# Kernel tuning notes

Measured on AMD Instinct MI355X. Metric: run time of the kernel, lower is better.

The kernel has to match this reference:

```python
import jax, jax.numpy as jnp
import numpy as np

N = 50000
E = 800000
D = 128
L = 2


def setup_inputs() -> dict:
    key = jax.random.key(0)
    k0, k1, k2 = jax.random.split(key, 3)
    x = jax.random.normal(k0, (N, D), dtype=jnp.float32)
    edge_index = jax.random.randint(k1, (2, E), 0, N, dtype=jnp.int64)
    # GCNConv weights: one [D, D] matrix + bias per layer (dim_in -> dim_in)
    W = jax.random.normal(k2, (L, D, D), dtype=jnp.float32) * (1.0 / np.sqrt(D))
    b = jnp.zeros((L, D), dtype=jnp.float32)
    return {"x": x, "edge_index": edge_index, "W": W, "b": b}


def reference(x, edge_index, W, b):
    """Stacked GCNConv + relu (dropout is identity in eval mode).

    GCNConv: out = D^{-1/2} (A + I) D^{-1/2} (X W) + b, with self-loops added.
    """
    n = x.shape[0]
    loops = jnp.arange(n, dtype=edge_index.dtype)
    src = jnp.concatenate([edge_index[0], loops])  # [E + N]
    dst = jnp.concatenate([edge_index[1], loops])  # [E + N]
    # Degree (with self-loops) based symmetric normalization
    deg = jax.ops.segment_sum(jnp.ones_like(dst, dtype=x.dtype), dst, num_segments=n)
    dinv = jax.lax.rsqrt(deg)  # deg >= 1 thanks to self-loops
    coef = (dinv[src] * dinv[dst])[:, None]  # [E + N, 1]

    num_layers = W.shape[0]
    for i in range(num_layers):
        h = x @ W[i]  # transform first, as PyG GCNConv does
        x = jax.ops.segment_sum(h[src] * coef, dst, num_segments=n) + b[i]
        x = jax.nn.relu(x)
        # F.dropout with training=False is identity
    return x
```

## Files before the change

### kernel.cpp

```cpp
#include <hip/hip_runtime.h>
#include <hip/hip_fp16.h>


#define D 128
#define SCAN_B 256
#define WP 136
#define ABI 6

typedef _Float16 half8 __attribute__((ext_vector_type(8)));
typedef float floatx4 __attribute__((ext_vector_type(4)));


__global__ void count_kernel(const int* __restrict__ dst, int* deg8,
                             int* __restrict__ rank, int e, int n) {
    int i = blockIdx.x * blockDim.x + threadIdx.x;
    int c = (blockIdx.x & 7) * n;
    if (i < e) rank[i] = atomicAdd(&deg8[c + dst[i]], 1);
}

__global__ __launch_bounds__(256) void scanA_cvtw_kernel(const int* __restrict__ deg8,
                                                         int* __restrict__ degT,
                                                         int* __restrict__ base8,
                                                         int* __restrict__ partial,
                                                         int n, int nbs,
                                                         const float* __restrict__ W,
                                                         __half* __restrict__ WhT) {
    __shared__ int red[4];
    int tid = threadIdx.x;
    int bid = blockIdx.x;
    if (bid < nbs) {
        int i = bid * 256 + tid;
        int tot = 0;
        if (i < n) {
            int run = 0;
#pragma unroll
            for (int c = 0; c < 8; ++c) {
                base8[c * n + i] = run;
                run += deg8[c * n + i];
            }
            degT[i] = run;
            tot = run;
        }
        for (int off = 32; off > 0; off >>= 1) tot += __shfl_down(tot, off, 64);
        if ((tid & 63) == 0) red[tid >> 6] = tot;
        __syncthreads();
        if (tid == 0) partial[bid] = red[0] + red[1] + red[2] + red[3];
    } else {
        int id = (bid - nbs) * 256 + tid;
        int l = id >> 14;
        int rem = id & 16383;
        int f = rem >> 7;
        int k = rem & 127;
        WhT[id] = __float2half(W[l * 16384 + k * 128 + f]);
    }
}

__global__ __launch_bounds__(256) void scanB_kernel(const int* __restrict__ partial,
                                                    int* __restrict__ blockoff, int nb) {
    __shared__ int sc[256];
    int tid = threadIdx.x;
    int c = (tid < nb) ? partial[tid] : 0;
    sc[tid] = c;
    __syncthreads();
    for (int off = 1; off < 256; off <<= 1) {
        int v = (tid >= off) ? sc[tid - off] : 0;
        __syncthreads();
        sc[tid] += v;
        __syncthreads();
    }
    if (tid <= nb) blockoff[tid] = (tid == 0) ? 0 : sc[tid - 1];
}

__global__ __launch_bounds__(SCAN_B) void scanC_kernel(const int* __restrict__ degT,
                                                       const int* __restrict__ blockoff,
                                                       int* __restrict__ row_ptr,
                                                       float* __restrict__ dinv,
                                                       int n, int nb) {
    __shared__ int sc[SCAN_B];
    int tid = threadIdx.x;
    int i = blockIdx.x * SCAN_B + tid;
    int c = (i < n) ? degT[i] : 0;
    sc[tid] = c;
    __syncthreads();
    for (int off = 1; off < SCAN_B; off <<= 1) {
        int v = (tid >= off) ? sc[tid - off] : 0;
        __syncthreads();
        sc[tid] += v;
        __syncthreads();
    }
    if (i < n) {
        int base = blockoff[blockIdx.x] + sc[tid] - c;
        row_ptr[i] = base;
        dinv[i] = rsqrtf((float)(c + 1));
    }
    if (blockIdx.x == 0 && tid == 0) row_ptr[n] = blockoff[nb];
}


__device__ inline void gemm_body(int bid, int tid,
                                 const float* __restrict__ Xf,
                                 const __half* __restrict__ Xh,
                                 const __half* __restrict__ WhT,
                                 __half* __restrict__ Hh, int n, int fromFloat,
                                 _Float16* wlds) {
#pragma unroll
    for (int q = 0; q < 8; ++q) {
        int idx = tid + q * 256;
        int row = idx >> 4;
        int col8 = (idx & 15) * 8;
        const uint2* gsrc = (const uint2*)(WhT + row * 128 + col8);
        uint2 a = gsrc[0];
        uint2 b = gsrc[1];
        uint2* ldst = (uint2*)(wlds + row * WP + col8);
        ldst[0] = a;
        ldst[1] = b;
    }
    __syncthreads();

    const int wave = tid >> 6;
    const int lane = tid & 63;
    const int m = lane & 15;
    const int quad = lane >> 4;

    const int node = bid * 64 + wave * 16 + m;
    const int node_ld = node < n ? node : (n - 1);

    half8 bfr[4];
    if (fromFloat) {
#pragma unroll
        for (int k = 0; k < 4; ++k) {
            const float4* p = (const float4*)(Xf + (size_t)node_ld * 128 + k * 32 + quad * 8);
            float4 lo = p[0];
            float4 hi = p[1];
            half8 h;
            h[0] = (_Float16)lo.x; h[1] = (_Float16)lo.y;
            h[2] = (_Float16)lo.z; h[3] = (_Float16)lo.w;
            h[4] = (_Float16)hi.x; h[5] = (_Float16)hi.y;
            h[6] = (_Float16)hi.z; h[7] = (_Float16)hi.w;
            bfr[k] = h;
        }
    } else {
#pragma unroll
        for (int k = 0; k < 4; ++k) {
            bfr[k] = *(const half8*)(Xh + (size_t)node_ld * 128 + k * 32 + quad * 8);
        }
    }

    floatx4 acc[8];
#pragma unroll
    for (int f = 0; f < 8; ++f) acc[f] = (floatx4){0.f, 0.f, 0.f, 0.f};

#pragma unroll
    for (int f = 0; f < 8; ++f) {
#pragma unroll
        for (int k = 0; k < 4; ++k) {
            half8 a = *(const half8*)(wlds + (f * 16 + m) * WP + k * 32 + quad * 8);
            acc[f] = __builtin_amdgcn_mfma_f32_16x16x32_f16(a, bfr[k], acc[f], 0, 0, 0);
        }
    }

    if (node < n) {
#pragma unroll
        for (int f = 0; f < 8; ++f) {
            __half2 p0 = __floats2half2_rn(acc[f][0], acc[f][1]);
            __half2 p1 = __floats2half2_rn(acc[f][2], acc[f][3]);
            uint2 pk;
            pk.x = *(unsigned int*)&p0;
            pk.y = *(unsigned int*)&p1;
            *(uint2*)(Hh + (size_t)node * 128 + f * 16 + quad * 4) = pk;
        }
    }
}

__device__ inline void fill_body(int i,
                                 const int* __restrict__ src,
                                 const int* __restrict__ dst,
                                 const int* __restrict__ rank,
                                 const int* __restrict__ row_ptr,
                                 const int* __restrict__ base8,
                                 const float* __restrict__ dinv,
                                 int2* __restrict__ recs, int e, int n) {
    if (i < e) {
        int d = dst[i];
        int s = src[i];
        int c = (i >> 8) & 7;
        int pos = row_ptr[d] + base8[c * n + d] + rank[i];
        int2 rec;
        rec.x = s;
        rec.y = __float_as_int(dinv[s] * dinv[d]);
        recs[pos] = rec;
    }
}


__global__ __launch_bounds__(256) void gemmfill_kernel(const float* __restrict__ Xf,
                                                       const __half* __restrict__ WhT,
                                                       __half* __restrict__ Hh, int n, int nbg,
                                                       const int* __restrict__ src,
                                                       const int* __restrict__ dst,
                                                       const int* __restrict__ rank,
                                                       const int* __restrict__ row_ptr,
                                                       const int* __restrict__ base8,
                                                       const float* __restrict__ dinv,
                                                       int2* __restrict__ recs, int e) {
    __shared__ _Float16 wlds[128 * WP];
    int bid = blockIdx.x;
    int tid = threadIdx.x;
    if (bid < nbg) {
        gemm_body(bid, tid, Xf, nullptr, WhT, Hh, n, 1, wlds);
    } else {
        fill_body((bid - nbg) * 256 + tid, src, dst, rank, row_ptr, base8, dinv, recs, e, n);
    }
}

__global__ __launch_bounds__(256) void gemm_f16in_kernel(const __half* __restrict__ Xh,
                                                         const __half* __restrict__ WhT,
                                                         __half* __restrict__ Hh, int n) {
    __shared__ _Float16 wlds[128 * WP];
    gemm_body(blockIdx.x, threadIdx.x, nullptr, Xh, WhT, Hh, n, 0, wlds);
}


__device__ inline void unpack8(uint4 u, float* f) {
    union { unsigned int x; __half2 h; } a, b, c, d;
    a.x = u.x; b.x = u.y; c.x = u.z; d.x = u.w;
    float2 f0 = __half22float2(a.h);
    float2 f1 = __half22float2(b.h);
    float2 f2 = __half22float2(c.h);
    float2 f3 = __half22float2(d.h);
    f[0] = f0.x; f[1] = f0.y; f[2] = f1.x; f[3] = f1.y;
    f[4] = f2.x; f[5] = f2.y; f[6] = f3.x; f[7] = f3.y;
}

__global__ __launch_bounds__(256) void agg_kernel(const __half* __restrict__ H,
                                                  const int2* __restrict__ recs,
                                                  const int* __restrict__ row_ptr,
                                                  const float* __restrict__ dinv,
                                                  const float* __restrict__ bias,
                                                  float* __restrict__ YF,
                                                  __half* __restrict__ YH,
                                                  int n, int writeHalf) {
    int wave = threadIdx.x >> 6;
    int lane = threadIdx.x & 63;
    int v = blockIdx.x * 4 + wave;
    if (v >= n) return;

    const int qw = lane >> 4;
    const int fl = lane & 15;
    const uint4* H16 = (const uint4*)H;

    float acc[8];
    {
        float di = dinv[v];
        float selfc = (qw == 0) ? di * di : 0.f;
        uint4 hv = H16[(size_t)v * 16 + fl];
        float f[8]; unpack8(hv, f);
#pragma unroll
        for (int t = 0; t < 8; ++t) acc[t] = f[t] * selfc;
    }

    int e0 = row_ptr[v];
    int e1 = row_ptr[v + 1];
    int e = e0;
    for (; e + 4 * ABI <= e1; e += 4 * ABI) {
        int2 r[ABI]; uint4 hu[ABI];
#pragma unroll
        for (int j = 0; j < ABI; ++j) r[j] = recs[e + 4 * j + qw];
#pragma unroll
        for (int j = 0; j < ABI; ++j) hu[j] = H16[(size_t)r[j].x * 16 + fl];
#pragma unroll
        for (int j = 0; j < ABI; ++j) {
            float c = __int_as_float(r[j].y);
            float f[8]; unpack8(hu[j], f);
#pragma unroll
            for (int t = 0; t < 8; ++t) acc[t] = fmaf(f[t], c, acc[t]);
        }
    }
    if (e < e1) {
        int2 r[ABI]; uint4 hu[ABI]; bool act[ABI];
#pragma unroll
        for (int j = 0; j < ABI; ++j) {
            int idx = e + 4 * j + qw;
            act[j] = idx < e1;
            if (act[j]) r[j] = recs[idx];
        }
#pragma unroll
        for (int j = 0; j < ABI; ++j) {
            if (act[j]) hu[j] = H16[(size_t)r[j].x * 16 + fl];
        }
#pragma unroll
        for (int j = 0; j < ABI; ++j) {
            if (act[j]) {
                float c = __int_as_float(r[j].y);
                float f[8]; unpack8(hu[j], f);
#pragma unroll
                for (int t = 0; t < 8; ++t) acc[t] = fmaf(f[t], c, acc[t]);
            }
        }
    }

#pragma unroll
    for (int t = 0; t < 8; ++t) {
        acc[t] += __shfl_xor(acc[t], 16);
        acc[t] += __shfl_xor(acc[t], 32);
    }

    if (qw == 0) {
        const float4* B4 = (const float4*)bias;
        float4 b0 = B4[fl * 2];
        float4 b1 = B4[fl * 2 + 1];
        float o[8];
        o[0] = fmaxf(acc[0] + b0.x, 0.f);
        o[1] = fmaxf(acc[1] + b0.y, 0.f);
        o[2] = fmaxf(acc[2] + b0.z, 0.f);
        o[3] = fmaxf(acc[3] + b0.w, 0.f);
        o[4] = fmaxf(acc[4] + b1.x, 0.f);
        o[5] = fmaxf(acc[5] + b1.y, 0.f);
        o[6] = fmaxf(acc[6] + b1.z, 0.f);
        o[7] = fmaxf(acc[7] + b1.w, 0.f);
        if (writeHalf) {
            __half2 p0 = __floats2half2_rn(o[0], o[1]);
            __half2 p1 = __floats2half2_rn(o[2], o[3]);
            __half2 p2 = __floats2half2_rn(o[4], o[5]);
            __half2 p3 = __floats2half2_rn(o[6], o[7]);
            uint4 pk;
            pk.x = *(unsigned int*)&p0;
            pk.y = *(unsigned int*)&p1;
            pk.z = *(unsigned int*)&p2;
            pk.w = *(unsigned int*)&p3;
            ((uint4*)YH)[(size_t)v * 16 + fl] = pk;
        } else {
            float4* Y4 = (float4*)YF;
            Y4[(size_t)v * 32 + fl * 2]     = make_float4(o[0], o[1], o[2], o[3]);
            Y4[(size_t)v * 32 + fl * 2 + 1] = make_float4(o[4], o[5], o[6], o[7]);
        }
    }
}


extern "C" void kernel_launch(void* const* d_in, const int* in_sizes, int n_in,
                              void* d_out, int out_size, void* d_ws, size_t ws_size,
                              hipStream_t stream) {
    const float* x = (const float*)d_in[0];
    const int* ei = (const int*)d_in[1];
    const float* W = (const float*)d_in[2];
    const float* b = (const float*)d_in[3];
    float* out = (float*)d_out;

    const int N = in_sizes[0] / D;
    const int E = in_sizes[1] / 2;

    const int* src = ei;
    const int* dst = ei + E;

    int* wsi = (int*)d_ws;
    float* wsf = (float*)d_ws;
    const size_t o_deg8 = 0;
    const size_t o_degT = o_deg8 + 400000;
    const size_t o_dinv = o_degT + 50000;
    const size_t o_rp   = o_dinv + 50000;
    const size_t o_part = o_rp + 50016;
    const size_t o_boff = o_part + 256;
    const size_t o_b8   = o_boff + 256;
    const size_t o_rank = o_b8 + 400000;
    const size_t o_rec  = o_rank + 800000;
    const size_t o_h    = o_rec + 1600000;
    const size_t o_wht  = o_h + 3200000;
    const size_t o_y1h  = o_wht + 16384;

    int* deg8    = wsi + o_deg8;
    int* degT    = wsi + o_degT;
    float* dinv  = wsf + o_dinv;
    int* row_ptr = wsi + o_rp;
    int* partial = wsi + o_part;
    int* blockoff= wsi + o_boff;
    int* base8   = wsi + o_b8;
    int* rank    = wsi + o_rank;
    int2* recs   = (int2*)(wsi + o_rec);
    __half* h    = (__half*)(wsi + o_h);
    __half* wht  = (__half*)(wsi + o_wht);
    __half* y1h  = (__half*)(wsi + o_y1h);

    const int nb_e = (E + 255) / 256;
    const int nb_s = (N + SCAN_B - 1) / SCAN_B;
    const int nb_g = (N + 63) / 64;
    const int nb_a = (N + 3) / 4;

    hipMemsetAsync(deg8, 0, (size_t)8 * 50000 * sizeof(int), stream);
    count_kernel<<<nb_e, 256, 0, stream>>>(dst, deg8, rank, E, N);
    scanA_cvtw_kernel<<<nb_s + 128, 256, 0, stream>>>(deg8, degT, base8, partial,
                                                      N, nb_s, W, wht);
    scanB_kernel<<<1, 256, 0, stream>>>(partial, blockoff, nb_s);
    scanC_kernel<<<nb_s, SCAN_B, 0, stream>>>(degT, blockoff, row_ptr, dinv, N, nb_s);
    gemmfill_kernel<<<nb_g + nb_e, 256, 0, stream>>>(x, wht, h, N, nb_g,
                                                     src, dst, rank, row_ptr, base8,
                                                     dinv, recs, E);
    agg_kernel<<<nb_a, 256, 0, stream>>>(h, recs, row_ptr, dinv, b, nullptr, y1h, N, 1);
    gemm_f16in_kernel<<<nb_g, 256, 0, stream>>>(y1h, wht + 16384, h, N);
    agg_kernel<<<nb_a, 256, 0, stream>>>(h, recs, row_ptr, dinv, b + D, out, nullptr, N, 0);
}
```

Measured before the change: 237.5 us.

## Fuse count, scans, and GEMM/fill into one persistent kernel with grid barriers

Replaces the count, three scan kernels and the gemm+fill kernel with a single persistent prep kernel of fixed grid size that uses atomic-counter grid barriers between phases. This removes four kernel launches and their inter-kernel gaps, and folds the block-offset scan into each block redundantly. It relies on all 768 blocks being co-resident (launch bounds 256,3) to avoid deadlock, and the GEMM and fill phases now loop over tiles with fewer blocks.

```diff
diff --git a/kernel.cpp b/kernel.cpp
--- a/kernel.cpp
+++ b/kernel.cpp
@@ -3,106 +3,29 @@
 
 
 #define D 128
-#define SCAN_B 256
 #define WP 136
 #define ABI 6
+#define GRID_PREP 768
+#define GB_G 384
+#define NB_SCAN 196
 
 typedef _Float16 half8 __attribute__((ext_vector_type(8)));
 typedef float floatx4 __attribute__((ext_vector_type(4)));
 
-
-__global__ void count_kernel(const int* __restrict__ dst, int* deg8,
-                             int* __restrict__ rank, int e, int n) {
-    int i = blockIdx.x * blockDim.x + threadIdx.x;
-    int c = (blockIdx.x & 7) * n;
-    if (i < e) rank[i] = atomicAdd(&deg8[c + dst[i]], 1);
-}
-
-__global__ __launch_bounds__(256) void scanA_cvtw_kernel(const int* __restrict__ deg8,
-                                                         int* __restrict__ degT,
-                                                         int* __restrict__ base8,
-                                                         int* __restrict__ partial,
-                                                         int n, int nbs,
-                                                         const float* __restrict__ W,
-                                                         __half* __restrict__ WhT) {
-    __shared__ int red[4];
-    int tid = threadIdx.x;
-    int bid = blockIdx.x;
-    if (bid < nbs) {
-        int i = bid * 256 + tid;
-        int tot = 0;
-        if (i < n) {
-            int run = 0;
-#pragma unroll
-            for (int c = 0; c < 8; ++c) {
-                base8[c * n + i] = run;
-                run += deg8[c * n + i];
-            }
-            degT[i] = run;
-            tot = run;
-        }
-        for (int off = 32; off > 0; off >>= 1) tot += __shfl_down(tot, off, 64);
-        if ((tid & 63) == 0) red[tid >> 6] = tot;
-        __syncthreads();
-        if (tid == 0) partial[bid] = red[0] + red[1] + red[2] + red[3];
-    } else {
-        int id = (bid - nbs) * 256 + tid;
-        int l = id >> 14;
-        int rem = id & 16383;
-        int f = rem >> 7;
-        int k = rem & 127;
-        WhT[id] = __float2half(W[l * 16384 + k * 128 + f]);
-    }
-}
-
-__global__ __launch_bounds__(256) void scanB_kernel(const int* __restrict__ partial,
-                                                    int* __restrict__ blockoff, int nb) {
-    __shared__ int sc[256];
-    int tid = threadIdx.x;
-    int c = (tid < nb) ? partial[tid] : 0;
-    sc[tid] = c;
+__device__ inline void gsync(int* ctr, int target) {
     __syncthreads();
-    for (int off = 1; off < 256; off <<= 1) {
-        int v = (tid >= off) ? sc[tid - off] : 0;
-        __syncthreads();
-        sc[tid] += v;
-        __syncthreads();
-    }
-    if (tid <= nb) blockoff[tid] = (tid == 0) ? 0 : sc[tid - 1];
-}
-
-__global__ __launch_bounds__(SCAN_B) void scanC_kernel(const int* __restrict__ degT,
-                                                       const int* __restrict__ blockoff,
-                                                       int* __restrict__ row_ptr,
-                                                       float* __restrict__ dinv,
-                                                       int n, int nb) {
-    __shared__ int sc[SCAN_B];
-    int tid = threadIdx.x;
-    int i = blockIdx.x * SCAN_B + tid;
-    int c = (i < n) ? degT[i] : 0;
-    sc[tid] = c;
+    if (threadIdx.x == 0) {
+        __threadfence();
+        atomicAdd(ctr, 1);
+        while (__hip_atomic_load(ctr, __ATOMIC_RELAXED, __HIP_MEMORY_SCOPE_AGENT) < target)
+            __builtin_amdgcn_s_sleep(2);
+        __threadfence();
+    }
     __syncthreads();
-    for (int off = 1; off < SCAN_B; off <<= 1) {
-        int v = (tid >= off) ? sc[tid - off] : 0;
-        __syncthreads();
-        sc[tid] += v;
-        __syncthreads();
-    }
-    if (i < n) {
-        int base = blockoff[blockIdx.x] + sc[tid] - c;
-        row_ptr[i] = base;
-        dinv[i] = rsqrtf((float)(c + 1));
-    }
-    if (blockIdx.x == 0 && tid == 0) row_ptr[n] = blockoff[nb];
-}
-
-
-__device__ inline void gemm_body(int bid, int tid,
-                                 const float* __restrict__ Xf,
-                                 const __half* __restrict__ Xh,
-                                 const __half* __restrict__ WhT,
-                                 __half* __restrict__ Hh, int n, int fromFloat,
-                                 _Float16* wlds) {
+}
+
+
+__device__ inline void stage_w(int tid, const __half* __restrict__ WhT, _Float16* wlds) {
 #pragma unroll
     for (int q = 0; q < 8; ++q) {
         int idx = tid + q * 256;
@@ -115,14 +38,19 @@
         ldst[0] = a;
         ldst[1] = b;
     }
-    __syncthreads();
-
+}
+
+__device__ inline void gemm_tile(int g, int tid,
+                                 const float* __restrict__ Xf,
+                                 const __half* __restrict__ Xh,
+                                 __half* __restrict__ Hh, int n, int fromFloat,
+                                 const _Float16* wlds) {
     const int wave = tid >> 6;
     const int lane = tid & 63;
     const int m = lane & 15;
     const int quad = lane >> 4;
 
-    const int node = bid * 64 + wave * 16 + m;
+    const int node = g * 64 + wave * 16 + m;
     const int node_ld = node < n ? node : (n - 1);
 
     half8 bfr[4];
@@ -170,6 +98,17 @@
             *(uint2*)(Hh + (size_t)node * 128 + f * 16 + quad * 4) = pk;
         }
     }
+}
+
+__device__ inline void gemm_body(int bid, int tid,
+                                 const float* __restrict__ Xf,
+                                 const __half* __restrict__ Xh,
+                                 const __half* __restrict__ WhT,
+                                 __half* __restrict__ Hh, int n, int fromFloat,
+                                 _Float16* wlds) {
+    stage_w(tid, WhT, wlds);
+    __syncthreads();
+    gemm_tile(bid, tid, Xf, Xh, Hh, n, fromFloat, wlds);
 }
 
 __device__ inline void fill_body(int i,
@@ -193,25 +132,92 @@
 }
 
 
-__global__ __launch_bounds__(256) void gemmfill_kernel(const float* __restrict__ Xf,
-                                                       const __half* __restrict__ WhT,
-                                                       __half* __restrict__ Hh, int n, int nbg,
-                                                       const int* __restrict__ src,
-                                                       const int* __restrict__ dst,
-                                                       const int* __restrict__ rank,
-                                                       const int* __restrict__ row_ptr,
-                                                       const int* __restrict__ base8,
-                                                       const float* __restrict__ dinv,
-                                                       int2* __restrict__ recs, int e) {
+__global__ __launch_bounds__(256, 3) void prep_kernel(
+    const int* __restrict__ src, const int* __restrict__ dst,
+    const float* __restrict__ x, const float* __restrict__ W,
+    int* __restrict__ deg8, int* __restrict__ base8,
+    int* __restrict__ partial,
+    int* __restrict__ row_ptr, float* __restrict__ dinv,
+    int* __restrict__ rank, int2* __restrict__ recs,
+    __half* __restrict__ WhT, __half* __restrict__ Hh,
+    int* ctr, int n, int e, int nbg) {
     __shared__ _Float16 wlds[128 * WP];
-    int bid = blockIdx.x;
-    int tid = threadIdx.x;
-    if (bid < nbg) {
-        gemm_body(bid, tid, Xf, nullptr, WhT, Hh, n, 1, wlds);
+    __shared__ int sc[256];
+    __shared__ int scb[256];
+    const int tid = threadIdx.x;
+    const int bid = blockIdx.x;
+    const int gid = bid * 256 + tid;
+
+    if (gid < 2 * D * D) {
+        int l = gid >> 14;
+        int rem = gid & 16383;
+        int f = rem >> 7;
+        int k = rem & 127;
+        WhT[gid] = __float2half(W[l * 16384 + k * 128 + f]);
+    }
+    for (int i = gid; i < e; i += GRID_PREP * 256) {
+        int c = (i >> 8) & 7;
+        rank[i] = atomicAdd(&deg8[c * n + dst[i]], 1);
+    }
+    gsync(ctr, GRID_PREP);
+
+    int mydeg = 0, myscan = 0;
+    if (bid < NB_SCAN) {
+        int i = gid;
+        if (i < n) {
+            int run = 0;
+#pragma unroll
+            for (int c = 0; c < 8; ++c) {
+                base8[c * n + i] = run;
+                run += deg8[c * n + i];
+            }
+            mydeg = run;
+        }
+        sc[tid] = mydeg;
+        __syncthreads();
+        for (int off = 1; off < 256; off <<= 1) {
+            int v = (tid >= off) ? sc[tid - off] : 0;
+            __syncthreads();
+            sc[tid] += v;
+            __syncthreads();
+        }
+        myscan = sc[tid];
+        if (tid == 255) partial[bid] = myscan;
+    }
+    gsync(ctr, 2 * GRID_PREP);
+
+    if (bid < NB_SCAN) {
+        int p = (tid < NB_SCAN) ? partial[tid] : 0;
+        scb[tid] = p;
+        __syncthreads();
+        for (int off = 1; off < 256; off <<= 1) {
+            int v = (tid >= off) ? scb[tid - off] : 0;
+            __syncthreads();
+            scb[tid] += v;
+            __syncthreads();
+        }
+        int boff = (bid == 0) ? 0 : scb[bid - 1];
+        int i = gid;
+        if (i < n) {
+            row_ptr[i] = boff + myscan - mydeg;
+            dinv[i] = rsqrtf((float)(mydeg + 1));
+        }
+        if (bid == 0 && tid == 0) row_ptr[n] = scb[NB_SCAN - 1];
+    }
+    gsync(ctr, 3 * GRID_PREP);
+
+    if (bid < GB_G) {
+        stage_w(tid, WhT, wlds);
+        __syncthreads();
+        for (int g = bid; g < nbg; g += GB_G)
+            gemm_tile(g, tid, x, nullptr, Hh, n, 1, wlds);
     } else {
-        fill_body((bid - nbg) * 256 + tid, src, dst, rank, row_ptr, base8, dinv, recs, e, n);
-    }
-}
+        const int FB = GRID_PREP - GB_G;
+        for (int i = (bid - GB_G) * 256 + tid; i < e; i += FB * 256)
+            fill_body(i, src, dst, rank, row_ptr, base8, dinv, recs, e, n);
+    }
+}
+
 
 __global__ __launch_bounds__(256) void gemm_f16in_kernel(const __half* __restrict__ Xh,
                                                          const __half* __restrict__ WhT,
@@ -356,12 +362,11 @@
     int* wsi = (int*)d_ws;
     float* wsf = (float*)d_ws;
     const size_t o_deg8 = 0;
-    const size_t o_degT = o_deg8 + 400000;
-    const size_t o_dinv = o_degT + 50000;
+    const size_t o_ctr  = o_deg8 + 400000;
+    const size_t o_dinv = o_ctr + 16;
     const size_t o_rp   = o_dinv + 50000;
     const size_t o_part = o_rp + 50016;
-    const size_t o_boff = o_part + 256;
-    const size_t o_b8   = o_boff + 256;
+    const size_t o_b8   = o_part + 256;
     const size_t o_rank = o_b8 + 400000;
     const size_t o_rec  = o_rank + 800000;
     const size_t o_h    = o_rec + 1600000;
@@ -369,11 +374,10 @@
     const size_t o_y1h  = o_wht + 16384;
 
     int* deg8    = wsi + o_deg8;
-    int* degT    = wsi + o_degT;
+    int* ctr     = wsi + o_ctr;
     float* dinv  = wsf + o_dinv;
     int* row_ptr = wsi + o_rp;
     int* partial = wsi + o_part;
-    int* blockoff= wsi + o_boff;
     int* base8   = wsi + o_b8;
     int* rank    = wsi + o_rank;
     int2* recs   = (int2*)(wsi + o_rec);
@@ -381,20 +385,13 @@
     __half* wht  = (__half*)(wsi + o_wht);
     __half* y1h  = (__half*)(wsi + o_y1h);
 
-    const int nb_e = (E + 255) / 256;
-    const int nb_s = (N + SCAN_B - 1) / SCAN_B;
     const int nb_g = (N + 63) / 64;
     const int nb_a = (N + 3) / 4;
 
-    hipMemsetAsync(deg8, 0, (size_t)8 * 50000 * sizeof(int), stream);
-    count_kernel<<<nb_e, 256, 0, stream>>>(dst, deg8, rank, E, N);
-    scanA_cvtw_kernel<<<nb_s + 128, 256, 0, stream>>>(deg8, degT, base8, partial,
-                                                      N, nb_s, W, wht);
-    scanB_kernel<<<1, 256, 0, stream>>>(partial, blockoff, nb_s);
-    scanC_kernel<<<nb_s, SCAN_B, 0, stream>>>(degT, blockoff, row_ptr, dinv, N, nb_s);
-    gemmfill_kernel<<<nb_g + nb_e, 256, 0, stream>>>(x, wht, h, N, nb_g,
-                                                     src, dst, rank, row_ptr, base8,
-                                                     dinv, recs, E);
+    hipMemsetAsync(deg8, 0, (size_t)(8 * 50000 + 16) * sizeof(int), stream);
+    prep_kernel<<<GRID_PREP, 256, 0, stream>>>(src, dst, x, W,
+                                               deg8, base8, partial, row_ptr, dinv,
+                                               rank, recs, wht, h, ctr, N, E, nb_g);
     agg_kernel<<<nb_a, 256, 0, stream>>>(h, recs, row_ptr, dinv, b, nullptr, y1h, N, 1);
     gemm_f16in_kernel<<<nb_g, 256, 0, stream>>>(y1h, wht + 16384, h, N);
     agg_kernel<<<nb_a, 256, 0, stream>>>(h, recs, row_ptr, dinv, b + D, out, nullptr, N, 0);
```

Measured after the change: 455.4 us. 1.92x slower.

## Fuse layer-1 aggregation with layer-2 GEMM and merge scan kernels

Applied to the files above, without the earlier changes.

Layer-1 aggregation and the layer-2 transform now run in one kernel. Each 512-thread block aggregates 64 nodes into an LDS tile and immediately multiplies it by the second weight matrix with MFMA. This removes the fp16 intermediate write/read round trip and one launch. Separately, the two-stage block-offset scan is folded into the row-pointer kernel, which hardcodes 196 scan blocks (valid only for N=50000) and saves another launch. The fused kernel serializes 8 rows per wave and reads the weights straight from global memory, so the aggregation may lose latency hiding.

```diff
diff --git a/kernel.cpp b/kernel.cpp
--- a/kernel.cpp
+++ b/kernel.cpp
@@ -3,9 +3,10 @@
 
 
 #define D 128
-#define SCAN_B 256
 #define WP 136
+#define YP 136
 #define ABI 6
+#define NB_SCAN 196
 
 typedef _Float16 half8 __attribute__((ext_vector_type(8)));
 typedef float floatx4 __attribute__((ext_vector_type(4)));
@@ -55,11 +56,25 @@
     }
 }
 
-__global__ __launch_bounds__(256) void scanB_kernel(const int* __restrict__ partial,
-                                                    int* __restrict__ blockoff, int nb) {
+__global__ __launch_bounds__(256) void scanC2_kernel(const int* __restrict__ degT,
+                                                     const int* __restrict__ partial,
+                                                     int* __restrict__ row_ptr,
+                                                     float* __restrict__ dinv, int n) {
     __shared__ int sc[256];
+    __shared__ int scb[256];
     int tid = threadIdx.x;
-    int c = (tid < nb) ? partial[tid] : 0;
+    int bid = blockIdx.x;
+    int p = (tid < NB_SCAN) ? partial[tid] : 0;
+    scb[tid] = p;
+    __syncthreads();
+    for (int off = 1; off < 256; off <<= 1) {
+        int v = (tid >= off) ? scb[tid - off] : 0;
+        __syncthreads();
+        scb[tid] += v;
+        __syncthreads();
+    }
+    int i = bid * 256 + tid;
+    int c = (i < n) ? degT[i] : 0;
     sc[tid] = c;
     __syncthreads();
     for (int off = 1; off < 256; off <<= 1) {
@@ -68,40 +83,19 @@
         sc[tid] += v;
         __syncthreads();
     }
-    if (tid <= nb) blockoff[tid] = (tid == 0) ? 0 : sc[tid - 1];
-}
-
-__global__ __launch_bounds__(SCAN_B) void scanC_kernel(const int* __restrict__ degT,
-                                                       const int* __restrict__ blockoff,
-                                                       int* __restrict__ row_ptr,
-                                                       float* __restrict__ dinv,
-                                                       int n, int nb) {
-    __shared__ int sc[SCAN_B];
-    int tid = threadIdx.x;
-    int i = blockIdx.x * SCAN_B + tid;
-    int c = (i < n) ? degT[i] : 0;
-    sc[tid] = c;
-    __syncthreads();
-    for (int off = 1; off < SCAN_B; off <<= 1) {
-        int v = (tid >= off) ? sc[tid - off] : 0;
-        __syncthreads();
-        sc[tid] += v;
-        __syncthreads();
-    }
     if (i < n) {
-        int base = blockoff[blockIdx.x] + sc[tid] - c;
+        int base = ((bid == 0) ? 0 : scb[bid - 1]) + sc[tid] - c;
         row_ptr[i] = base;
         dinv[i] = rsqrtf((float)(c + 1));
     }
-    if (blockIdx.x == 0 && tid == 0) row_ptr[n] = blockoff[nb];
+    if (bid == 0 && tid == 0) row_ptr[n] = scb[NB_SCAN - 1];
 }
 
 
 __device__ inline void gemm_body(int bid, int tid,
                                  const float* __restrict__ Xf,
-                                 const __half* __restrict__ Xh,
                                  const __half* __restrict__ WhT,
-                                 __half* __restrict__ Hh, int n, int fromFloat,
+                                 __half* __restrict__ Hh, int n,
                                  _Float16* wlds) {
 #pragma unroll
     for (int q = 0; q < 8; ++q) {
@@ -126,24 +120,17 @@
     const int node_ld = node < n ? node : (n - 1);
 
     half8 bfr[4];
-    if (fromFloat) {
-#pragma unroll
-        for (int k = 0; k < 4; ++k) {
-            const float4* p = (const float4*)(Xf + (size_t)node_ld * 128 + k * 32 + quad * 8);
-            float4 lo = p[0];
-            float4 hi = p[1];
-            half8 h;
-            h[0] = (_Float16)lo.x; h[1] = (_Float16)lo.y;
-            h[2] = (_Float16)lo.z; h[3] = (_Float16)lo.w;
-            h[4] = (_Float16)hi.x; h[5] = (_Float16)hi.y;
-            h[6] = (_Float16)hi.z; h[7] = (_Float16)hi.w;
-            bfr[k] = h;
-        }
-    } else {
-#pragma unroll
-        for (int k = 0; k < 4; ++k) {
-            bfr[k] = *(const half8*)(Xh + (size_t)node_ld * 128 + k * 32 + quad * 8);
-        }
+#pragma unroll
+    for (int k = 0; k < 4; ++k) {
+        const float4* p = (const float4*)(Xf + (size_t)node_ld * 128 + k * 32 + quad * 8);
+        float4 lo = p[0];
+        float4 hi = p[1];
+        half8 h;
+        h[0] = (_Float16)lo.x; h[1] = (_Float16)lo.y;
+        h[2] = (_Float16)lo.z; h[3] = (_Float16)lo.w;
+        h[4] = (_Float16)hi.x; h[5] = (_Float16)hi.y;
+        h[6] = (_Float16)hi.z; h[7] = (_Float16)hi.w;
+        bfr[k] = h;
     }
 
     floatx4 acc[8];
@@ -207,17 +194,10 @@
     int bid = blockIdx.x;
     int tid = threadIdx.x;
     if (bid < nbg) {
-        gemm_body(bid, tid, Xf, nullptr, WhT, Hh, n, 1, wlds);
+        gemm_body(bid, tid, Xf, WhT, Hh, n, wlds);
     } else {
         fill_body((bid - nbg) * 256 + tid, src, dst, rank, row_ptr, base8, dinv, recs, e, n);
     }
-}
-
-__global__ __launch_bounds__(256) void gemm_f16in_kernel(const __half* __restrict__ Xh,
-                                                         const __half* __restrict__ WhT,
-                                                         __half* __restrict__ Hh, int n) {
-    __shared__ _Float16 wlds[128 * WP];
-    gemm_body(blockIdx.x, threadIdx.x, nullptr, Xh, WhT, Hh, n, 0, wlds);
 }
 
 
@@ -232,14 +212,68 @@
     f[4] = f2.x; f[5] = f2.y; f[6] = f3.x; f[7] = f3.y;
 }
 
+__device__ inline void agg_row(int v, int qw, int fl,
+                               const uint4* __restrict__ H16,
+                               const int2* __restrict__ recs,
+                               const int* __restrict__ row_ptr,
+                               const float* __restrict__ dinv,
+                               float* acc) {
+    {
+        float di = dinv[v];
+        float selfc = (qw == 0) ? di * di : 0.f;
+        uint4 hv = H16[(size_t)v * 16 + fl];
+        float f[8]; unpack8(hv, f);
+#pragma unroll
+        for (int t = 0; t < 8; ++t) acc[t] = f[t] * selfc;
+    }
+
+    int e0 = row_ptr[v];
+    int e1 = row_ptr[v + 1];
+    int e = e0;
+    for (; e + 4 * ABI <= e1; e += 4 * ABI) {
+        int2 r[ABI]; uint4 hu[ABI];
+#pragma unroll
+        for (int j = 0; j < ABI; ++j) r[j] = recs[e + 4 * j + qw];
+#pragma unroll
+        for (int j = 0; j < ABI; ++j) hu[j] = H16[(size_t)r[j].x * 16 + fl];
+#pragma unroll
+        for (int j = 0; j < ABI; ++j) {
+            float c = __int_as_float(r[j].y);
+            float f[8]; unpack8(hu[j], f);
+#pragma unroll
+            for (int t = 0; t < 8; ++t) acc[t] = fmaf(f[t], c, acc[t]);
+        }
+    }
+    if (e < e1) {
+        int2 r[ABI]; uint4 hu[ABI]; bool act[ABI];
+#pragma unroll
+        for (int j = 0; j < ABI; ++j) {
+            int idx = e + 4 * j + qw;
+            act[j] = idx < e1;
+            if (act[j]) r[j] = recs[idx];
+        }
+#pragma unroll
+        for (int j = 0; j < ABI; ++j) {
+            if (act[j]) hu[j] = H16[(size_t)r[j].x * 16 + fl];
+        }
+#pragma unroll
+        for (int j = 0; j < ABI; ++j) {
+            if (act[j]) {
+                float c = __int_as_float(r[j].y);
+                float f[8]; unpack8(hu[j], f);
+#pragma unroll
+                for (int t = 0; t < 8; ++t) acc[t] = fmaf(f[t], c, acc[t]);
+            }
+        }
+    }
+}
+
 __global__ __launch_bounds__(256) void agg_kernel(const __half* __restrict__ H,
                                                   const int2* __restrict__ recs,
                                                   const int* __restrict__ row_ptr,
                                                   const float* __restrict__ dinv,
                                                   const float* __restrict__ bias,
-                                                  float* __restrict__ YF,
-                                                  __half* __restrict__ YH,
-                                                  int n, int writeHalf) {
+                                                  float* __restrict__ YF, int n) {
     int wave = threadIdx.x >> 6;
     int lane = threadIdx.x & 63;
     int v = blockIdx.x * 4 + wave;
@@ -250,54 +284,7 @@
     const uint4* H16 = (const uint4*)H;
 
     float acc[8];
-    {
-        float di = dinv[v];
-        float selfc = (qw == 0) ? di * di : 0.f;
-        uint4 hv = H16[(size_t)v * 16 + fl];
-        float f[8]; unpack8(hv, f);
-#pragma unroll
-        for (int t = 0; t < 8; ++t) acc[t] = f[t] * selfc;
-    }
-
-    int e0 = row_ptr[v];
-    int e1 = row_ptr[v + 1];
-    int e = e0;
-    for (; e + 4 * ABI <= e1; e += 4 * ABI) {
-        int2 r[ABI]; uint4 hu[ABI];
-#pragma unroll
-        for (int j = 0; j < ABI; ++j) r[j] = recs[e + 4 * j + qw];
-#pragma unroll
-        for (int j = 0; j < ABI; ++j) hu[j] = H16[(size_t)r[j].x * 16 + fl];
-#pragma unroll
-        for (int j = 0; j < ABI; ++j) {
-            float c = __int_as_float(r[j].y);
-            float f[8]; unpack8(hu[j], f);
-#pragma unroll
-            for (int t = 0; t < 8; ++t) acc[t] = fmaf(f[t], c, acc[t]);
-        }
-    }
-    if (e < e1) {
-        int2 r[ABI]; uint4 hu[ABI]; bool act[ABI];
-#pragma unroll
-        for (int j = 0; j < ABI; ++j) {
-            int idx = e + 4 * j + qw;
-            act[j] = idx < e1;
-            if (act[j]) r[j] = recs[idx];
-        }
-#pragma unroll
-        for (int j = 0; j < ABI; ++j) {
-            if (act[j]) hu[j] = H16[(size_t)r[j].x * 16 + fl];
-        }
-#pragma unroll
-        for (int j = 0; j < ABI; ++j) {
-            if (act[j]) {
-                float c = __int_as_float(r[j].y);
-                float f[8]; unpack8(hu[j], f);
-#pragma unroll
-                for (int t = 0; t < 8; ++t) acc[t] = fmaf(f[t], c, acc[t]);
-            }
-        }
-    }
+    agg_row(v, qw, fl, H16, recs, row_ptr, dinv, acc);
 
 #pragma unroll
     for (int t = 0; t < 8; ++t) {
@@ -309,30 +296,92 @@
         const float4* B4 = (const float4*)bias;
         float4 b0 = B4[fl * 2];
         float4 b1 = B4[fl * 2 + 1];
-        float o[8];
-        o[0] = fmaxf(acc[0] + b0.x, 0.f);
-        o[1] = fmaxf(acc[1] + b0.y, 0.f);
-        o[2] = fmaxf(acc[2] + b0.z, 0.f);
-        o[3] = fmaxf(acc[3] + b0.w, 0.f);
-        o[4] = fmaxf(acc[4] + b1.x, 0.f);
-        o[5] = fmaxf(acc[5] + b1.y, 0.f);
-        o[6] = fmaxf(acc[6] + b1.z, 0.f);
-        o[7] = fmaxf(acc[7] + b1.w, 0.f);
-        if (writeHalf) {
-            __half2 p0 = __floats2half2_rn(o[0], o[1]);
-            __half2 p1 = __floats2half2_rn(o[2], o[3]);
-            __half2 p2 = __floats2half2_rn(o[4], o[5]);
-            __half2 p3 = __floats2half2_rn(o[6], o[7]);
-            uint4 pk;
+        float4* Y4 = (float4*)YF;
+        Y4[(size_t)v * 32 + fl * 2] = make_float4(
+            fmaxf(acc[0] + b0.x, 0.f), fmaxf(acc[1] + b0.y, 0.f),
+            fmaxf(acc[2] + b0.z, 0.f), fmaxf(acc[3] + b0.w, 0.f));
+        Y4[(size_t)v * 32 + fl * 2 + 1] = make_float4(
+            fmaxf(acc[4] + b1.x, 0.f), fmaxf(acc[5] + b1.y, 0.f),
+            fmaxf(acc[6] + b1.z, 0.f), fmaxf(acc[7] + b1.w, 0.f));
+    }
+}
+
+__global__ __launch_bounds__(512, 4) void aggemm_kernel(
+    const __half* __restrict__ H,
+    const int2* __restrict__ recs,
+    const int* __restrict__ row_ptr,
+    const float* __restrict__ dinv,
+    const float* __restrict__ bias,
+    const __half* __restrict__ WhT2,
+    __half* __restrict__ H2, int n) {
+    __shared__ _Float16 yt[64 * YP];
+    const int tid = threadIdx.x;
+    const int wave = tid >> 6;
+    const int lane = tid & 63;
+    const int qw = lane >> 4;
+    const int fl = lane & 15;
+    const int g = blockIdx.x;
+    const uint4* H16 = (const uint4*)H;
+
+    const float4* B4 = (const float4*)bias;
+    float4 b0 = B4[fl * 2];
+    float4 b1 = B4[fl * 2 + 1];
+#pragma unroll 1
+    for (int it = 0; it < 8; ++it) {
+        int r = wave * 8 + it;
+        int v = g * 64 + r;
+        if (v < n) {
+            float acc[8];
+            agg_row(v, qw, fl, H16, recs, row_ptr, dinv, acc);
+#pragma unroll
+            for (int t = 0; t < 8; ++t) {
+                acc[t] += __shfl_xor(acc[t], 16);
+                acc[t] += __shfl_xor(acc[t], 32);
+            }
+            if (qw == 0) {
+                __half2 p0 = __floats2half2_rn(fmaxf(acc[0] + b0.x, 0.f), fmaxf(acc[1] + b0.y, 0.f));
+                __half2 p1 = __floats2half2_rn(fmaxf(acc[2] + b0.z, 0.f), fmaxf(acc[3] + b0.w, 0.f));
+                __half2 p2 = __floats2half2_rn(fmaxf(acc[4] + b1.x, 0.f), fmaxf(acc[5] + b1.y, 0.f));
+                __half2 p3 = __floats2half2_rn(fmaxf(acc[6] + b1.z, 0.f), fmaxf(acc[7] + b1.w, 0.f));
+                uint4 pk;
+                pk.x = *(unsigned int*)&p0;
+                pk.y = *(unsigned int*)&p1;
+                pk.z = *(unsigned int*)&p2;
+                pk.w = *(unsigned int*)&p3;
+                *(uint4*)&yt[r * YP + fl * 8] = pk;
+            }
+        } else if (qw == 0) {
+            uint4 z = make_uint4(0, 0, 0, 0);
+            *(uint4*)&yt[r * YP + fl * 8] = z;
+        }
+    }
+    __syncthreads();
+
+    const int mg = wave & 3;
+    const int fh = wave >> 2;
+    const int node = g * 64 + mg * 16 + fl;
+
+    half8 bfr[4];
+#pragma unroll
+    for (int k = 0; k < 4; ++k)
+        bfr[k] = *(const half8*)&yt[(mg * 16 + fl) * YP + k * 32 + qw * 8];
+
+#pragma unroll
+    for (int fb = 0; fb < 4; ++fb) {
+        int f = fh * 4 + fb;
+        floatx4 a4 = (floatx4){0.f, 0.f, 0.f, 0.f};
+#pragma unroll
+        for (int k = 0; k < 4; ++k) {
+            half8 a = *(const half8*)(WhT2 + ((f * 16 + fl) * 128 + k * 32 + qw * 8));
+            a4 = __builtin_amdgcn_mfma_f32_16x16x32_f16(a, bfr[k], a4, 0, 0, 0);
+        }
+        if (node < n) {
+            __half2 p0 = __floats2half2_rn(a4[0], a4[1]);
+            __half2 p1 = __floats2half2_rn(a4[2], a4[3]);
+            uint2 pk;
             pk.x = *(unsigned int*)&p0;
             pk.y = *(unsigned int*)&p1;
-            pk.z = *(unsigned int*)&p2;
-            pk.w = *(unsigned int*)&p3;
-            ((uint4*)YH)[(size_t)v * 16 + fl] = pk;
-        } else {
-            float4* Y4 = (float4*)YF;
-            Y4[(size_t)v * 32 + fl * 2]     = make_float4(o[0], o[1], o[2], o[3]);
-            Y4[(size_t)v * 32 + fl * 2 + 1] = make_float4(o[4], o[5], o[6], o[7]);
+            *(uint2*)(H2 + (size_t)node * 128 + f * 16 + qw * 4) = pk;
         }
     }
 }
@@ -366,23 +415,22 @@
     const size_t o_rec  = o_rank + 800000;
     const size_t o_h    = o_rec + 1600000;
     const size_t o_wht  = o_h + 3200000;
-    const size_t o_y1h  = o_wht + 16384;
+    const size_t o_h2   = o_wht + 16384;
 
     int* deg8    = wsi + o_deg8;
     int* degT    = wsi + o_degT;
     float* dinv  = wsf + o_dinv;
     int* row_ptr = wsi + o_rp;
     int* partial = wsi + o_part;
-    int* blockoff= wsi + o_boff;
     int* base8   = wsi + o_b8;
     int* rank    = wsi + o_rank;
     int2* recs   = (int2*)(wsi + o_rec);
     __half* h    = (__half*)(wsi + o_h);
     __half* wht  = (__half*)(wsi + o_wht);
-    __half* y1h  = (__half*)(wsi + o_y1h);
+    __half* h2   = (__half*)(wsi + o_h2);
 
     const int nb_e = (E + 255) / 256;
-    const int nb_s = (N + SCAN_B - 1) / SCAN_B;
+    const int nb_s = (N + 255) / 256;
     const int nb_g = (N + 63) / 64;
     const int nb_a = (N + 3) / 4;
 
@@ -390,12 +438,11 @@
     count_kernel<<<nb_e, 256, 0, stream>>>(dst, deg8, rank, E, N);
     scanA_cvtw_kernel<<<nb_s + 128, 256, 0, stream>>>(deg8, degT, base8, partial,
                                                       N, nb_s, W, wht);
-    scanB_kernel<<<1, 256, 0, stream>>>(partial, blockoff, nb_s);
-    scanC_kernel<<<nb_s, SCAN_B, 0, stream>>>(degT, blockoff, row_ptr, dinv, N, nb_s);
+    scanC2_kernel<<<nb_s, 256, 0, stream>>>(degT, partial, row_ptr, dinv, N);
     gemmfill_kernel<<<nb_g + nb_e, 256, 0, stream>>>(x, wht, h, N, nb_g,
                                                      src, dst, rank, row_ptr, base8,
                                                      dinv, recs, E);
-    agg_kernel<<<nb_a, 256, 0, stream>>>(h, recs, row_ptr, dinv, b, nullptr, y1h, N, 1);
-    gemm_f16in_kernel<<<nb_g, 256, 0, stream>>>(y1h, wht + 16384, h, N);
-    agg_kernel<<<nb_a, 256, 0, stream>>>(h, recs, row_ptr, dinv, b + D, out, nullptr, N, 0);
-}
+    aggemm_kernel<<<nb_g, 512, 0, stream>>>(h, recs, row_ptr, dinv, b,
+                                            wht + 16384, h2, N);
+    agg_kernel<<<nb_a, 256, 0, stream>>>(h2, recs, row_ptr, dinv, b + D, out, N);
+}
```

Measured after the change: 244.5 us. 3.0% more time.
